# Kernel tuning notes

Hardware: AMD Instinct MI355X
Metric: run time of the kernel (lower is better)

## Reference

```python
import jax, jax.numpy as jnp
import numpy as np

B, S, D = 8, 1024, 1152
H = 16
HD = D // H
HID = int(D * 4.0)
LN_EPS = 1e-5


def layer_norm(x, w, b):
    m = jnp.mean(x, axis=-1, keepdims=True)
    v = jnp.mean(jnp.square(x - m), axis=-1, keepdims=True)
    return (x - m) * jax.lax.rsqrt(v + LN_EPS) * w + b


def modulate(x, shift, scale):
    # shift/scale: [B, D] broadcast over seq
    return x * (1.0 + scale[:, None, :]) + shift[:, None, :]


def setup_inputs() -> dict:
    key = jax.random.key(0)
    ks = jax.random.split(key, 16)
    s = 0.02
    return {
        "x": jax.random.normal(ks[0], (B, S, D), jnp.float32),
        "c": jax.random.normal(ks[1], (B, D), jnp.float32),
        "ln1_w": jnp.ones((D,), jnp.float32),
        "ln1_b": jnp.zeros((D,), jnp.float32),
        "wq": jax.random.normal(ks[2], (D, D), jnp.float32) * s,
        "wk": jax.random.normal(ks[3], (D, D), jnp.float32) * s,
        "wv": jax.random.normal(ks[4], (D, D), jnp.float32) * s,
        "wo": jax.random.normal(ks[5], (D, D), jnp.float32) * s,
        "wo_b": jnp.zeros((D,), jnp.float32),
        "ln2_w": jnp.ones((D,), jnp.float32),
        "ln2_b": jnp.zeros((D,), jnp.float32),
        "fc1_w": jax.random.normal(ks[6], (D, HID), jnp.float32) * s,
        "fc1_b": jnp.zeros((HID,), jnp.float32),
        "fc2_w": jax.random.normal(ks[7], (HID, D), jnp.float32) * s,
        "fc2_b": jnp.zeros((D,), jnp.float32),
        "ada_w": jax.random.normal(ks[8], (D, 6 * D), jnp.float32) * s,
        "ada_b": jnp.zeros((6 * D,), jnp.float32),
    }


def attention(x, wq, wk, wv, wo, wo_b):
    b, s, d = x.shape
    q = (x @ wq).reshape(b, s, H, HD).transpose(0, 2, 1, 3)  # [B,H,S,hd]
    k = (x @ wk).reshape(b, s, H, HD).transpose(0, 2, 1, 3)
    v = (x @ wv).reshape(b, s, H, HD).transpose(0, 2, 1, 3)
    scale = 1.0 / np.sqrt(HD).astype(np.float32)
    att = jnp.einsum("bhqd,bhkd->bhqk", q, k) * scale
    att = jax.nn.softmax(att, axis=-1)
    out = jnp.einsum("bhqk,bhkd->bhqd", att, v)
    out = out.transpose(0, 2, 1, 3).reshape(b, s, d)
    return out @ wo + wo_b


def reference(x, c, ln1_w, ln1_b, wq, wk, wv, wo, wo_b, ln2_w, ln2_b,
              fc1_w, fc1_b, fc2_w, fc2_b, ada_w, ada_b):
    mod = jax.nn.silu(c) @ ada_w + ada_b  # [B, 6D]
    sh_msa, sc_msa, g_msa, sh_mlp, sc_mlp, g_mlp = jnp.split(mod, 6, axis=1)
    h = modulate(layer_norm(x, ln1_w, ln1_b), sh_msa, sc_msa)
    x = x + g_msa[:, None, :] * attention(h, wq, wk, wv, wo, wo_b)
    h = modulate(layer_norm(x, ln2_w, ln2_b), sh_mlp, sc_mlp)
    h = jax.nn.gelu(h @ fc1_w + fc1_b, approximate=False) @ fc2_w + fc2_b
    x = x + g_mlp[:, None, :] * h
    return x
```

## Files before the change

kernel.cpp:

```cpp
#include <hip/hip_runtime.h>
#include <hip/hip_bf16.h>


typedef unsigned short u16;
typedef unsigned int u32;
typedef __attribute__((ext_vector_type(8))) short bf16x8;
typedef __attribute__((ext_vector_type(4))) float f32x4;
typedef __attribute__((ext_vector_type(16))) float f32x16;

#define MFMA16(a, b, c) __builtin_amdgcn_mfma_f32_16x16x32_bf16((a), (b), (c), 0, 0, 0)
#define MFMA32(a, b, c) __builtin_amdgcn_mfma_f32_32x32x16_bf16((a), (b), (c), 0, 0, 0)

__device__ __forceinline__ u16 f2bf(float f) {
  __hip_bfloat16 h = __float2bfloat16(f);
  return __builtin_bit_cast(u16, h);
}

__device__ __forceinline__ float bf2f(u16 u) {
  u32 v = ((u32)u) << 16;
  return __builtin_bit_cast(float, v);
}

__device__ __forceinline__ void gload16(const u16* g, u16* l) {
  __builtin_amdgcn_global_load_lds(
      (const __attribute__((address_space(1))) unsigned int*)(const void*)g,
      (__attribute__((address_space(3))) unsigned int*)(void*)l, 16, 0, 0);
}

__global__ __launch_bounds__(256) void k_modproj1(const float* __restrict__ cc,
                                                  const float* __restrict__ aw,
                                                  float* __restrict__ partial) {
  __shared__ float lc[8][144];
  int kc = blockIdx.y;
  for (int i = threadIdx.x; i < 1152; i += 256) {
    int b = i / 144, k = i % 144;
    float v = cc[b * 1152 + kc * 144 + k];
    lc[b][k] = v / (1.f + __expf(-v));
  }
  __syncthreads();
  int j = blockIdx.x * 256 + threadIdx.x;
  float acc[8] = {0, 0, 0, 0, 0, 0, 0, 0};
  for (int k = 0; k < 144; ++k) {
    float w = aw[(size_t)(kc * 144 + k) * 6912 + j];
    #pragma unroll
    for (int b = 0; b < 8; ++b) acc[b] += lc[b][k] * w;
  }
  #pragma unroll
  for (int b = 0; b < 8; ++b) partial[((size_t)kc * 8 + b) * 6912 + j] = acc[b];
}

__global__ __launch_bounds__(256) void k_modproj2(const float* __restrict__ partial,
                                                  const float* __restrict__ ab,
                                                  float* __restrict__ mo) {
  int j = blockIdx.x * 256 + threadIdx.x;
  float bias = ab[j];
  #pragma unroll
  for (int b = 0; b < 8; ++b) {
    float s = 0.f;
    #pragma unroll
    for (int kc = 0; kc < 8; ++kc) s += partial[((size_t)kc * 8 + b) * 6912 + j];
    mo[(size_t)b * 6912 + j] = s + bias;
  }
}

__global__ __launch_bounds__(256) void k_tcvt(const float* __restrict__ in, u16* __restrict__ out,
                                              int K, int N) {
  __shared__ float t[32][33];
  int tx = threadIdx.x & 31, ty = threadIdx.x >> 5;
  size_t bx = (size_t)blockIdx.x * 32, by = (size_t)blockIdx.y * 32;
  #pragma unroll
  for (int i = 0; i < 4; ++i) t[ty + 8 * i][tx] = in[(by + ty + 8 * i) * N + bx + tx];
  __syncthreads();
  #pragma unroll
  for (int i = 0; i < 4; ++i) out[(bx + ty + 8 * i) * K + by + tx] = f2bf(t[tx][ty + 8 * i]);
}

__global__ __launch_bounds__(256) void k_lnmod(const float* __restrict__ xin,
                                               const float* __restrict__ w,
                                               const float* __restrict__ bs,
                                               const float* __restrict__ mo,
                                               int sh_off, int sc_off, u16* __restrict__ o) {
  int row = blockIdx.x;
  int b = row >> 10;
  int tid = threadIdx.x;
  const float4* x4 = (const float4*)(xin + (size_t)row * 1152);
  float4 v0 = x4[tid];
  float4 v1 = make_float4(0.f, 0.f, 0.f, 0.f);
  if (tid < 32) v1 = x4[256 + tid];
  float s = v0.x + v0.y + v0.z + v0.w + v1.x + v1.y + v1.z + v1.w;
  float sq = v0.x * v0.x + v0.y * v0.y + v0.z * v0.z + v0.w * v0.w +
             v1.x * v1.x + v1.y * v1.y + v1.z * v1.z + v1.w * v1.w;
  #pragma unroll
  for (int d = 32; d > 0; d >>= 1) { s += __shfl_down(s, d); sq += __shfl_down(sq, d); }
  __shared__ float ps[4], pq[4];
  int wid = tid >> 6, lane = tid & 63;
  if (lane == 0) { ps[wid] = s; pq[wid] = sq; }
  __syncthreads();
  float S = ps[0] + ps[1] + ps[2] + ps[3];
  float SQ = pq[0] + pq[1] + pq[2] + pq[3];
  float mean = S * (1.f / 1152.f);
  float var = SQ * (1.f / 1152.f) - mean * mean;
  float rs = rsqrtf(var + 1e-5f);
  const float* shp = mo + (size_t)b * 6912 + sh_off;
  const float* scp = mo + (size_t)b * 6912 + sc_off;
  u16* orow = o + (size_t)row * 1152;
  {
    int col = 4 * tid;
    ushort4 u; float y;
    y = (v0.x - mean) * rs * w[col + 0] + bs[col + 0]; u.x = f2bf(y * (1.f + scp[col + 0]) + shp[col + 0]);
    y = (v0.y - mean) * rs * w[col + 1] + bs[col + 1]; u.y = f2bf(y * (1.f + scp[col + 1]) + shp[col + 1]);
    y = (v0.z - mean) * rs * w[col + 2] + bs[col + 2]; u.z = f2bf(y * (1.f + scp[col + 2]) + shp[col + 2]);
    y = (v0.w - mean) * rs * w[col + 3] + bs[col + 3]; u.w = f2bf(y * (1.f + scp[col + 3]) + shp[col + 3]);
    *(ushort4*)&orow[col] = u;
  }
  if (tid < 32) {
    int col = 1024 + 4 * tid;
    ushort4 u; float y;
    y = (v1.x - mean) * rs * w[col + 0] + bs[col + 0]; u.x = f2bf(y * (1.f + scp[col + 0]) + shp[col + 0]);
    y = (v1.y - mean) * rs * w[col + 1] + bs[col + 1]; u.y = f2bf(y * (1.f + scp[col + 1]) + shp[col + 1]);
    y = (v1.z - mean) * rs * w[col + 2] + bs[col + 2]; u.z = f2bf(y * (1.f + scp[col + 2]) + shp[col + 2]);
    y = (v1.w - mean) * rs * w[col + 3] + bs[col + 3]; u.w = f2bf(y * (1.f + scp[col + 3]) + shp[col + 3]);
    *(ushort4*)&orow[col] = u;
  }
}

template <int EPI>
__global__ __launch_bounds__(256) void k_gemm(const u16* __restrict__ A, const u16* __restrict__ Bt,
                                              int Kst, int klen, u16* __restrict__ Cb,
                                              float* __restrict__ Cf,
                                              const float* __restrict__ bias,
                                              const float* __restrict__ res,
                                              const float* __restrict__ mo, int goff,
                                              u16* __restrict__ vt) {
  const int tid = threadIdx.x;
  const int w = tid >> 6, lane = tid & 63;
  const int wr = w >> 1, wc = w & 1;
  const int l31 = lane & 31, hi = lane >> 5;

  const int nwg = gridDim.x * gridDim.y;
  const int id = blockIdx.y * gridDim.x + blockIdx.x;
  const int swz = (id & 7) * (nwg >> 3) + (id >> 3);
  const int tM = (swz / gridDim.x) * 128, tN = (swz % gridDim.x) * 128;
  const int N = gridDim.x * 128;
  const int koff = blockIdx.z * klen;

  __shared__ u16 lA[2][128 * 32];
  __shared__ u16 lB[2][128 * 32];
  f32x16 acc[2][2];
  #pragma unroll
  for (int m = 0; m < 2; ++m)
    #pragma unroll
    for (int n = 0; n < 2; ++n)
      #pragma unroll
      for (int r = 0; r < 16; ++r) acc[m][n][r] = 0.f;

  const int lrow = lane >> 2, lseg = lane & 3;
  const int fl = (lrow & 3) ^ ((lrow >> 2) & 3);
  const u16* gA = A + (size_t)(tM + w * 32 + lrow) * Kst + (lseg ^ fl) * 8 + koff;
  const u16* gB = Bt + (size_t)(tN + w * 32 + lrow) * Kst + (lseg ^ fl) * 8 + koff;
  const size_t rstep = (size_t)16 * Kst;
  const int wo0 = (w * 32) * 32, wo1 = (w * 32 + 16) * 32;
  const int fr = (l31 & 3) ^ ((l31 >> 2) & 3);
  const int c0 = (hi ^ fr) * 8;
  const int c1 = ((hi ^ fr) ^ 2) * 8;
  const int arow = (wr * 64 + l31) * 32;
  const int brow = (wc * 64 + l31) * 32;

#define STAGE(buf, ks)                        \
  do {                                        \
    gload16(gA + (ks), lA[buf] + wo0);        \
    gload16(gA + rstep + (ks), lA[buf] + wo1);\
    gload16(gB + (ks), lB[buf] + wo0);        \
    gload16(gB + rstep + (ks), lB[buf] + wo1);\
  } while (0)

#define COMPUTE(buf)                                                            \
  do {                                                                          \
    bf16x8 a00 = *(const bf16x8*)&lA[buf][arow + c0];                           \
    bf16x8 a01 = *(const bf16x8*)&lA[buf][arow + c1];                           \
    bf16x8 a10 = *(const bf16x8*)&lA[buf][arow + 1024 + c0];                    \
    bf16x8 a11 = *(const bf16x8*)&lA[buf][arow + 1024 + c1];                    \
    bf16x8 b00 = *(const bf16x8*)&lB[buf][brow + c0];                           \
    bf16x8 b01 = *(const bf16x8*)&lB[buf][brow + c1];                           \
    bf16x8 b10 = *(const bf16x8*)&lB[buf][brow + 1024 + c0];                    \
    bf16x8 b11 = *(const bf16x8*)&lB[buf][brow + 1024 + c1];                    \
    acc[0][0] = MFMA32(a00, b00, acc[0][0]);                                    \
    acc[0][1] = MFMA32(a00, b10, acc[0][1]);                                    \
    acc[1][0] = MFMA32(a10, b00, acc[1][0]);                                    \
    acc[1][1] = MFMA32(a10, b10, acc[1][1]);                                    \
    acc[0][0] = MFMA32(a01, b01, acc[0][0]);                                    \
    acc[0][1] = MFMA32(a01, b11, acc[0][1]);                                    \
    acc[1][0] = MFMA32(a11, b01, acc[1][0]);                                    \
    acc[1][1] = MFMA32(a11, b11, acc[1][1]);                                    \
  } while (0)

  const int nt = klen >> 5;
  STAGE(0, 0);
  __syncthreads();
  int t = 1;
  for (; t + 1 < nt; t += 2) {
    STAGE(1, t * 32);
    COMPUTE(0);
    __syncthreads();
    STAGE(0, t * 32 + 32);
    COMPUTE(1);
    __syncthreads();
  }
  STAGE(1, t * 32);
  COMPUTE(0);
  __syncthreads();
  COMPUTE(1);
#undef STAGE
#undef COMPUTE

  #pragma unroll
  for (int m = 0; m < 2; ++m)
    #pragma unroll
    for (int n = 0; n < 2; ++n) {
      int gcol = tN + wc * 64 + n * 32 + l31;
      #pragma unroll
      for (int q = 0; q < 4; ++q) {
        int grow0 = tM + wr * 64 + m * 32 + hi * 4 + q * 8;
        if (EPI == 3) {
          if (tN < 2304) {
            #pragma unroll
            for (int r = 0; r < 4; ++r)
              Cb[(size_t)(grow0 + r) * N + gcol] = f2bf(acc[m][n][q * 4 + r]);
          } else {
            int qq = gcol - 2304;
            int hh = qq / 72;
            int d = qq - hh * 72;
            int bb = grow0 >> 10, sl = grow0 & 1023;
            ushort4 u;
            u.x = f2bf(acc[m][n][q * 4 + 0]); u.y = f2bf(acc[m][n][q * 4 + 1]);
            u.z = f2bf(acc[m][n][q * 4 + 2]); u.w = f2bf(acc[m][n][q * 4 + 3]);
            *(ushort4*)&vt[(((size_t)bb * 16 + hh) * 72 + d) * 1024 + sl] = u;
          }
        } else if (EPI == 5) {
          u16* Po = Cb + (size_t)blockIdx.z * ((size_t)gridDim.y * 128) * N;
          #pragma unroll
          for (int r = 0; r < 4; ++r)
            Po[(size_t)(grow0 + r) * N + gcol] = f2bf(acc[m][n][q * 4 + r]);
        } else if (EPI == 1) {
          float g = mo[(size_t)(grow0 >> 10) * 6912 + goff + gcol];
          float bi = bias[gcol];
          #pragma unroll
          for (int r = 0; r < 4; ++r) {
            size_t idx = (size_t)(grow0 + r) * N + gcol;
            Cf[idx] = res[idx] + g * (acc[m][n][q * 4 + r] + bi);
          }
        } else {
          float bi = bias[gcol];
          #pragma unroll
          for (int r = 0; r < 4; ++r) {
            float z = acc[m][n][q * 4 + r] + bi;
            float z2 = z * z;
            float u = z * __fmaf_rn(z2, -0.0713548162f, -1.5957691216f);
            float e = __expf(u);
            Cb[(size_t)(grow0 + r) * N + gcol] = f2bf(z * __builtin_amdgcn_rcpf(1.f + e));
          }
        }
      }
    }
}

__global__ __launch_bounds__(256) void k_fc2red(const u16* __restrict__ p,
                                                const float* __restrict__ x1,
                                                const float* __restrict__ bias,
                                                const float* __restrict__ mo,
                                                float* __restrict__ out) {
  size_t i = ((size_t)blockIdx.x * 256 + threadIdx.x) * 4;
  int row = (int)(i / 1152);
  int col = (int)(i - (size_t)row * 1152);
  int b = row >> 10;
  ushort4 a0 = *(const ushort4*)(p + i);
  ushort4 a1 = *(const ushort4*)(p + 9437184ull + i);
  float4 r = *(const float4*)(x1 + i);
  const float* gp = mo + (size_t)b * 6912 + 5760 + col;
  const float* bp = bias + col;
  float4 o;
  o.x = r.x + gp[0] * (bf2f(a0.x) + bf2f(a1.x) + bp[0]);
  o.y = r.y + gp[1] * (bf2f(a0.y) + bf2f(a1.y) + bp[1]);
  o.z = r.z + gp[2] * (bf2f(a0.z) + bf2f(a1.z) + bp[2]);
  o.w = r.w + gp[3] * (bf2f(a0.w) + bf2f(a1.w) + bp[3]);
  *(float4*)(out + i) = o;
}

__global__ __launch_bounds__(256) void k_attn(const u16* __restrict__ QKV, const u16* __restrict__ Vt,
                                              u16* __restrict__ O) {
  const int tid = threadIdx.x;
  const int w = tid >> 6, lane = tid & 63;
  const int lr = lane & 15, kg = lane >> 4;
  int bx = blockIdx.x;
  bx = (bx & 7) * 256 + (bx >> 3);
  const int qt = bx & 15, h = (bx >> 4) & 15, b = bx >> 8;

  __shared__ u16 lQ[64][104];
  __shared__ u16 lK[64][104];
  __shared__ u16 lVt[80][72];
  __shared__ u16 lPt[4][16][72];

  const size_t qkbase = (size_t)b * 1024 * 3456 + (size_t)h * 72;
  const u16* Qg = QKV + qkbase;
  const u16* Kg = QKV + qkbase + 1152;
  const u16* Vg = Vt + ((size_t)(b * 16 + h) * 72) * 1024;

  const uint4 z4 = make_uint4(0, 0, 0, 0);
  for (int L = tid; L < 192; L += 256) {
    int r = L / 3, s = L - (L / 3) * 3;
    *(uint4*)&lQ[r][72 + s * 8] = z4;
    *(uint4*)&lK[r][72 + s * 8] = z4;
  }
  for (int L = tid; L < 72; L += 256) {
    int r = L / 9, s = L - (L / 9) * 9;
    *(uint4*)&lVt[72 + r][s * 8] = z4;
  }
  {
    int L = tid; int r = L / 9, s = L - r * 9;
    *(uint4*)&lQ[r][s * 8] = *(const uint4*)(Qg + (size_t)(qt * 64 + r) * 3456 + s * 8);
    L = tid + 256; r = L / 9; s = L - r * 9;
    *(uint4*)&lQ[r][s * 8] = *(const uint4*)(Qg + (size_t)(qt * 64 + r) * 3456 + s * 8);
    if (tid < 64) {
      L = tid + 512; r = L / 9; s = L - r * 9;
      *(uint4*)&lQ[r][s * 8] = *(const uint4*)(Qg + (size_t)(qt * 64 + r) * 3456 + s * 8);
    }
  }
  __syncthreads();

  bf16x8 bq[3];
  #pragma unroll
  for (int ks = 0; ks < 3; ++ks) bq[ks] = *(const bf16x8*)&lQ[w * 16 + lr][ks * 32 + kg * 8];

  const float scale = 0.11785113019775793f;
  float mrun = -1e30f, lrun = 0.f;
  f32x4 oacc[5];
  #pragma unroll
  for (int nd = 0; nd < 5; ++nd) oacc[nd] = f32x4{0.f, 0.f, 0.f, 0.f};

  for (int kt = 0; kt < 16; ++kt) {
    __syncthreads();
    {
      int L = tid; int r = L / 9, s = L - (L / 9) * 9;
      *(uint4*)&lK[r][s * 8] = *(const uint4*)(Kg + (size_t)(kt * 64 + r) * 3456 + s * 8);
      int d = tid >> 3, sg = tid & 7;
      *(uint4*)&lVt[d][sg * 8] = *(const uint4*)(Vg + (size_t)d * 1024 + kt * 64 + sg * 8);
      L = tid + 256; r = L / 9; s = L - r * 9;
      *(uint4*)&lK[r][s * 8] = *(const uint4*)(Kg + (size_t)(kt * 64 + r) * 3456 + s * 8);
      d = (tid + 256) >> 3; sg = tid & 7;
      *(uint4*)&lVt[d][sg * 8] = *(const uint4*)(Vg + (size_t)d * 1024 + kt * 64 + sg * 8);
      if (tid < 64) {
        L = tid + 512; r = L / 9; s = L - r * 9;
        *(uint4*)&lK[r][s * 8] = *(const uint4*)(Kg + (size_t)(kt * 64 + r) * 3456 + s * 8);
        d = (tid + 512) >> 3;
        *(uint4*)&lVt[d][sg * 8] = *(const uint4*)(Vg + (size_t)d * 1024 + kt * 64 + sg * 8);
      }
    }
    __syncthreads();

    f32x4 sfr[4];
    __builtin_amdgcn_s_setprio(1);
    #pragma unroll
    for (int kb = 0; kb < 4; ++kb) {
      f32x4 sv = f32x4{0.f, 0.f, 0.f, 0.f};
      #pragma unroll
      for (int ks = 0; ks < 3; ++ks) {
        bf16x8 ak = *(const bf16x8*)&lK[kb * 16 + lr][ks * 32 + kg * 8];
        sv = MFMA16(ak, bq[ks], sv);
      }
      sfr[kb] = sv;
    }
    __builtin_amdgcn_s_setprio(0);

    float mx = sfr[0][0];
    #pragma unroll
    for (int kb = 0; kb < 4; ++kb)
      #pragma unroll
      for (int r = 0; r < 4; ++r) mx = fmaxf(mx, sfr[kb][r]);
    mx = fmaxf(mx, __shfl_xor(mx, 16));
    mx = fmaxf(mx, __shfl_xor(mx, 32));
    mx *= scale;
    float mn = fmaxf(mrun, mx);
    float al = __expf(mrun - mn);
    mrun = mn;
    float sum = 0.f;
    #pragma unroll
    for (int kb = 0; kb < 4; ++kb) {
      #pragma unroll
      for (int rp = 0; rp < 2; ++rp) {
        float p0 = __expf(__fmaf_rn(sfr[kb][2 * rp], scale, -mn));
        float p1 = __expf(__fmaf_rn(sfr[kb][2 * rp + 1], scale, -mn));
        sum += p0 + p1;
        u32 pk = (u32)f2bf(p0) | ((u32)f2bf(p1) << 16);
        *(u32*)&lPt[w][lr][kb * 16 + kg * 4 + rp * 2] = pk;
      }
    }
    sum += __shfl_xor(sum, 16);
    sum += __shfl_xor(sum, 32);
    lrun = lrun * al + sum;
    #pragma unroll
    for (int nd = 0; nd < 5; ++nd)
      #pragma unroll
      for (int r = 0; r < 4; ++r) oacc[nd][r] *= al;

    __builtin_amdgcn_s_setprio(1);
    #pragma unroll
    for (int s = 0; s < 2; ++s) {
      bf16x8 bp = *(const bf16x8*)&lPt[w][lr][s * 32 + kg * 8];
      #pragma unroll
      for (int nd = 0; nd < 5; ++nd) {
        bf16x8 av = *(const bf16x8*)&lVt[nd * 16 + lr][s * 32 + kg * 8];
        oacc[nd] = MFMA16(av, bp, oacc[nd]);
      }
    }
    __builtin_amdgcn_s_setprio(0);
  }

  float inv = 1.f / lrun;
  size_t orow = ((size_t)b * 1024 + qt * 64 + w * 16 + lr) * 1152 + h * 72;
  #pragma unroll
  for (int nd = 0; nd < 5; ++nd) {
    int d0 = nd * 16 + kg * 4;
    if (d0 < 72) {
      ushort4 u;
      u.x = f2bf(oacc[nd][0] * inv);
      u.y = f2bf(oacc[nd][1] * inv);
      u.z = f2bf(oacc[nd][2] * inv);
      u.w = f2bf(oacc[nd][3] * inv);
      *(ushort4*)&O[orow + d0] = u;
    }
  }
}

extern "C" void kernel_launch(void* const* d_in, const int* in_sizes, int n_in,
                              void* d_out, int out_size, void* d_ws, size_t ws_size,
                              hipStream_t stream) {
  const float* x     = (const float*)d_in[0];
  const float* c     = (const float*)d_in[1];
  const float* ln1_w = (const float*)d_in[2];
  const float* ln1_b = (const float*)d_in[3];
  const float* wq    = (const float*)d_in[4];
  const float* wk    = (const float*)d_in[5];
  const float* wv    = (const float*)d_in[6];
  const float* wo    = (const float*)d_in[7];
  const float* wo_b  = (const float*)d_in[8];
  const float* ln2_w = (const float*)d_in[9];
  const float* ln2_b = (const float*)d_in[10];
  const float* fc1_w = (const float*)d_in[11];
  const float* fc1_b = (const float*)d_in[12];
  const float* fc2_w = (const float*)d_in[13];
  const float* fc2_b = (const float*)d_in[14];
  const float* ada_w = (const float*)d_in[15];
  const float* ada_b = (const float*)d_in[16];
  float* out = (float*)d_out;

  char* base = (char*)d_ws;
  size_t off = 0;
  auto alloc = [&](size_t nbytes) -> void* {
    void* p = base + off;
    off += (nbytes + 255) & ~(size_t)255;
    return p;
  };
  const size_t MD = 8192ull * 1152;
  float* partial = (float*)alloc(64ull * 6912 * 4);
  float* modb   = (float*)alloc(55296 * 4);
  u16* qkvT = (u16*)alloc(3456ull * 1152 * 2);
  u16* woT  = (u16*)alloc(1152ull * 1152 * 2);
  u16* fc1T = (u16*)alloc(4608ull * 1152 * 2);
  u16* fc2T = (u16*)alloc(1152ull * 4608 * 2);
  u16* hbuf = (u16*)alloc(MD * 2);
  float* x1 = (float*)alloc(MD * 4);
  u16* vtb  = (u16*)alloc(128ull * 72 * 1024 * 2);
  u16* fc2p = (u16*)alloc(2ull * MD * 2);
  u16* big  = (u16*)alloc(8192ull * 4608 * 2);
  u16* qkv = big;
  u16* m1 = big;

  k_modproj1<<<dim3(27, 8), 256, 0, stream>>>(c, ada_w, partial);
  k_modproj2<<<27, 256, 0, stream>>>(partial, ada_b, modb);
  k_tcvt<<<dim3(36, 36), 256, 0, stream>>>(wq, qkvT, 1152, 1152);
  k_tcvt<<<dim3(36, 36), 256, 0, stream>>>(wk, qkvT + 1152ull * 1152, 1152, 1152);
  k_tcvt<<<dim3(36, 36), 256, 0, stream>>>(wv, qkvT + 2304ull * 1152, 1152, 1152);
  k_tcvt<<<dim3(36, 36), 256, 0, stream>>>(wo, woT, 1152, 1152);
  k_tcvt<<<dim3(144, 36), 256, 0, stream>>>(fc1_w, fc1T, 1152, 4608);
  k_tcvt<<<dim3(36, 144), 256, 0, stream>>>(fc2_w, fc2T, 4608, 1152);

  k_lnmod<<<8192, 256, 0, stream>>>(x, ln1_w, ln1_b, modb, 0, 1152, hbuf);
  k_gemm<3><<<dim3(27, 64), 256, 0, stream>>>(hbuf, qkvT, 1152, 1152, qkv, nullptr, nullptr, nullptr, nullptr, 0, vtb);
  k_attn<<<2048, 256, 0, stream>>>(qkv, vtb, hbuf);
  k_gemm<1><<<dim3(9, 64), 256, 0, stream>>>(hbuf, woT, 1152, 1152, nullptr, x1, wo_b, x, modb, 2304, nullptr);
  k_lnmod<<<8192, 256, 0, stream>>>(x1, ln2_w, ln2_b, modb, 3456, 4608, hbuf);
  k_gemm<2><<<dim3(36, 64), 256, 0, stream>>>(hbuf, fc1T, 1152, 1152, m1, nullptr, fc1_b, nullptr, nullptr, 0, nullptr);
  k_gemm<5><<<dim3(9, 64, 2), 256, 0, stream>>>(m1, fc2T, 4608, 2304, fc2p, nullptr, nullptr, nullptr, nullptr, 0, nullptr);
  k_fc2red<<<9216, 256, 0, stream>>>(fc2p, x1, fc2_b, modb, out);
}
```

Before: 583.6 us.

## Widen GEMM tiles to 128x256 with each wave owning a 64-column strip

Changes the GEMM block tile from 128x128 to 128x256. Each of the four waves now computes 128 rows by 64 columns with 4x2 MFMA accumulators, which raises register use and LDS for B but improves operand reuse per LDS load. Weight buffers and the fc2 partial buffer are padded to multiples of 256 columns, and epilogues guard out-of-range columns. The wider tile halves the grid size, which may hurt wave occupancy and load balance on the narrower GEMMs. Padded weight rows are left uninitialised, but their outputs are either discarded or never read.

Result: slower. 625.1 us (+7.1%).

```diff
diff --git a/kernel.cpp b/kernel.cpp
--- a/kernel.cpp
+++ b/kernel.cpp
@@ -126,29 +126,27 @@
 
 template <int EPI>
 __global__ __launch_bounds__(256) void k_gemm(const u16* __restrict__ A, const u16* __restrict__ Bt,
-                                              int Kst, int klen, u16* __restrict__ Cb,
-                                              float* __restrict__ Cf,
+                                              int Kst, int klen, int NC,
+                                              u16* __restrict__ Cb, float* __restrict__ Cf,
                                               const float* __restrict__ bias,
                                               const float* __restrict__ res,
                                               const float* __restrict__ mo, int goff,
                                               u16* __restrict__ vt) {
   const int tid = threadIdx.x;
   const int w = tid >> 6, lane = tid & 63;
-  const int wr = w >> 1, wc = w & 1;
   const int l31 = lane & 31, hi = lane >> 5;
 
   const int nwg = gridDim.x * gridDim.y;
   const int id = blockIdx.y * gridDim.x + blockIdx.x;
   const int swz = (id & 7) * (nwg >> 3) + (id >> 3);
-  const int tM = (swz / gridDim.x) * 128, tN = (swz % gridDim.x) * 128;
-  const int N = gridDim.x * 128;
+  const int tM = (swz / gridDim.x) * 128, tN = (swz % gridDim.x) * 256;
   const int koff = blockIdx.z * klen;
 
   __shared__ u16 lA[2][128 * 32];
-  __shared__ u16 lB[2][128 * 32];
-  f32x16 acc[2][2];
-  #pragma unroll
-  for (int m = 0; m < 2; ++m)
+  __shared__ u16 lB[2][256 * 32];
+  f32x16 acc[4][2];
+  #pragma unroll
+  for (int m = 0; m < 4; ++m)
     #pragma unroll
     for (int n = 0; n < 2; ++n)
       #pragma unroll
@@ -157,41 +155,47 @@
   const int lrow = lane >> 2, lseg = lane & 3;
   const int fl = (lrow & 3) ^ ((lrow >> 2) & 3);
   const u16* gA = A + (size_t)(tM + w * 32 + lrow) * Kst + (lseg ^ fl) * 8 + koff;
-  const u16* gB = Bt + (size_t)(tN + w * 32 + lrow) * Kst + (lseg ^ fl) * 8 + koff;
+  const u16* gB = Bt + (size_t)(tN + w * 64 + lrow) * Kst + (lseg ^ fl) * 8 + koff;
   const size_t rstep = (size_t)16 * Kst;
-  const int wo0 = (w * 32) * 32, wo1 = (w * 32 + 16) * 32;
+  const int a0 = (w * 32) * 32, a1 = (w * 32 + 16) * 32;
+  const int b0 = (w * 64) * 32, b1 = (w * 64 + 16) * 32;
+  const int b2 = (w * 64 + 32) * 32, b3 = (w * 64 + 48) * 32;
   const int fr = (l31 & 3) ^ ((l31 >> 2) & 3);
   const int c0 = (hi ^ fr) * 8;
   const int c1 = ((hi ^ fr) ^ 2) * 8;
-  const int arow = (wr * 64 + l31) * 32;
-  const int brow = (wc * 64 + l31) * 32;
-
-#define STAGE(buf, ks)                        \
-  do {                                        \
-    gload16(gA + (ks), lA[buf] + wo0);        \
-    gload16(gA + rstep + (ks), lA[buf] + wo1);\
-    gload16(gB + (ks), lB[buf] + wo0);        \
-    gload16(gB + rstep + (ks), lB[buf] + wo1);\
+  const int arow = l31 * 32;
+  const int brow = (w * 64 + l31) * 32;
+
+#define STAGE(buf, ks)                                 \
+  do {                                                 \
+    gload16(gA + (ks), lA[buf] + a0);                  \
+    gload16(gA + rstep + (ks), lA[buf] + a1);          \
+    gload16(gB + (ks), lB[buf] + b0);                  \
+    gload16(gB + rstep + (ks), lB[buf] + b1);          \
+    gload16(gB + 2 * rstep + (ks), lB[buf] + b2);      \
+    gload16(gB + 3 * rstep + (ks), lB[buf] + b3);      \
   } while (0)
 
-#define COMPUTE(buf)                                                            \
-  do {                                                                          \
-    bf16x8 a00 = *(const bf16x8*)&lA[buf][arow + c0];                           \
-    bf16x8 a01 = *(const bf16x8*)&lA[buf][arow + c1];                           \
-    bf16x8 a10 = *(const bf16x8*)&lA[buf][arow + 1024 + c0];                    \
-    bf16x8 a11 = *(const bf16x8*)&lA[buf][arow + 1024 + c1];                    \
-    bf16x8 b00 = *(const bf16x8*)&lB[buf][brow + c0];                           \
-    bf16x8 b01 = *(const bf16x8*)&lB[buf][brow + c1];                           \
-    bf16x8 b10 = *(const bf16x8*)&lB[buf][brow + 1024 + c0];                    \
-    bf16x8 b11 = *(const bf16x8*)&lB[buf][brow + 1024 + c1];                    \
-    acc[0][0] = MFMA32(a00, b00, acc[0][0]);                                    \
-    acc[0][1] = MFMA32(a00, b10, acc[0][1]);                                    \
-    acc[1][0] = MFMA32(a10, b00, acc[1][0]);                                    \
-    acc[1][1] = MFMA32(a10, b10, acc[1][1]);                                    \
-    acc[0][0] = MFMA32(a01, b01, acc[0][0]);                                    \
-    acc[0][1] = MFMA32(a01, b11, acc[0][1]);                                    \
-    acc[1][0] = MFMA32(a11, b01, acc[1][0]);                                    \
-    acc[1][1] = MFMA32(a11, b11, acc[1][1]);                                    \
+#define COMPUTE(buf)                                                                 \
+  do {                                                                               \
+    bf16x8 afr[4][2], bfr[2][2];                                                     \
+    _Pragma("unroll")                                                                \
+    for (int m = 0; m < 4; ++m) {                                                    \
+      afr[m][0] = *(const bf16x8*)&lA[buf][arow + m * 1024 + c0];                    \
+      afr[m][1] = *(const bf16x8*)&lA[buf][arow + m * 1024 + c1];                    \
+    }                                                                                \
+    _Pragma("unroll")                                                                \
+    for (int n = 0; n < 2; ++n) {                                                    \
+      bfr[n][0] = *(const bf16x8*)&lB[buf][brow + n * 1024 + c0];                    \
+      bfr[n][1] = *(const bf16x8*)&lB[buf][brow + n * 1024 + c1];                    \
+    }                                                                                \
+    _Pragma("unroll")                                                                \
+    for (int m = 0; m < 4; ++m)                                                      \
+      _Pragma("unroll")                                                              \
+      for (int n = 0; n < 2; ++n) {                                                  \
+        acc[m][n] = MFMA32(afr[m][0], bfr[n][0], acc[m][n]);                         \
+        acc[m][n] = MFMA32(afr[m][1], bfr[n][1], acc[m][n]);                         \
+      }                                                                              \
   } while (0)
 
   const int nt = klen >> 5;
@@ -214,19 +218,19 @@
 #undef COMPUTE
 
   #pragma unroll
-  for (int m = 0; m < 2; ++m)
+  for (int m = 0; m < 4; ++m)
     #pragma unroll
     for (int n = 0; n < 2; ++n) {
-      int gcol = tN + wc * 64 + n * 32 + l31;
+      int gcol = tN + w * 64 + n * 32 + l31;
       #pragma unroll
       for (int q = 0; q < 4; ++q) {
-        int grow0 = tM + wr * 64 + m * 32 + hi * 4 + q * 8;
+        int grow0 = tM + m * 32 + hi * 4 + q * 8;
         if (EPI == 3) {
-          if (tN < 2304) {
+          if (gcol < 2304) {
             #pragma unroll
             for (int r = 0; r < 4; ++r)
-              Cb[(size_t)(grow0 + r) * N + gcol] = f2bf(acc[m][n][q * 4 + r]);
-          } else {
+              Cb[(size_t)(grow0 + r) * 3456 + gcol] = f2bf(acc[m][n][q * 4 + r]);
+          } else if (gcol < 3456) {
             int qq = gcol - 2304;
             int hh = qq / 72;
             int d = qq - hh * 72;
@@ -237,17 +241,19 @@
             *(ushort4*)&vt[(((size_t)bb * 16 + hh) * 72 + d) * 1024 + sl] = u;
           }
         } else if (EPI == 5) {
-          u16* Po = Cb + (size_t)blockIdx.z * ((size_t)gridDim.y * 128) * N;
+          u16* Po = Cb + (size_t)blockIdx.z * ((size_t)gridDim.y * 128) * NC;
           #pragma unroll
           for (int r = 0; r < 4; ++r)
-            Po[(size_t)(grow0 + r) * N + gcol] = f2bf(acc[m][n][q * 4 + r]);
+            Po[(size_t)(grow0 + r) * NC + gcol] = f2bf(acc[m][n][q * 4 + r]);
         } else if (EPI == 1) {
-          float g = mo[(size_t)(grow0 >> 10) * 6912 + goff + gcol];
-          float bi = bias[gcol];
-          #pragma unroll
-          for (int r = 0; r < 4; ++r) {
-            size_t idx = (size_t)(grow0 + r) * N + gcol;
-            Cf[idx] = res[idx] + g * (acc[m][n][q * 4 + r] + bi);
+          if (gcol < 1152) {
+            float g = mo[(size_t)(grow0 >> 10) * 6912 + goff + gcol];
+            float bi = bias[gcol];
+            #pragma unroll
+            for (int r = 0; r < 4; ++r) {
+              size_t idx = (size_t)(grow0 + r) * 1152 + gcol;
+              Cf[idx] = res[idx] + g * (acc[m][n][q * 4 + r] + bi);
+            }
           }
         } else {
           float bi = bias[gcol];
@@ -257,7 +263,7 @@
             float z2 = z * z;
             float u = z * __fmaf_rn(z2, -0.0713548162f, -1.5957691216f);
             float e = __expf(u);
-            Cb[(size_t)(grow0 + r) * N + gcol] = f2bf(z * __builtin_amdgcn_rcpf(1.f + e));
+            Cb[(size_t)(grow0 + r) * NC + gcol] = f2bf(z * __builtin_amdgcn_rcpf(1.f + e));
           }
         }
       }
@@ -273,8 +279,9 @@
   int row = (int)(i / 1152);
   int col = (int)(i - (size_t)row * 1152);
   int b = row >> 10;
-  ushort4 a0 = *(const ushort4*)(p + i);
-  ushort4 a1 = *(const ushort4*)(p + 9437184ull + i);
+  size_t pi = (size_t)row * 1280 + col;
+  ushort4 a0 = *(const ushort4*)(p + pi);
+  ushort4 a1 = *(const ushort4*)(p + 10485760ull + pi);
   float4 r = *(const float4*)(x1 + i);
   const float* gp = mo + (size_t)b * 6912 + 5760 + col;
   const float* bp = bias + col;
@@ -463,14 +470,14 @@
   const size_t MD = 8192ull * 1152;
   float* partial = (float*)alloc(64ull * 6912 * 4);
   float* modb   = (float*)alloc(55296 * 4);
-  u16* qkvT = (u16*)alloc(3456ull * 1152 * 2);
-  u16* woT  = (u16*)alloc(1152ull * 1152 * 2);
+  u16* qkvT = (u16*)alloc(3584ull * 1152 * 2);
+  u16* woT  = (u16*)alloc(1280ull * 1152 * 2);
   u16* fc1T = (u16*)alloc(4608ull * 1152 * 2);
-  u16* fc2T = (u16*)alloc(1152ull * 4608 * 2);
+  u16* fc2T = (u16*)alloc(1280ull * 4608 * 2);
   u16* hbuf = (u16*)alloc(MD * 2);
   float* x1 = (float*)alloc(MD * 4);
   u16* vtb  = (u16*)alloc(128ull * 72 * 1024 * 2);
-  u16* fc2p = (u16*)alloc(2ull * MD * 2);
+  u16* fc2p = (u16*)alloc(2ull * 8192 * 1280 * 2);
   u16* big  = (u16*)alloc(8192ull * 4608 * 2);
   u16* qkv = big;
   u16* m1 = big;
@@ -485,11 +492,11 @@
   k_tcvt<<<dim3(36, 144), 256, 0, stream>>>(fc2_w, fc2T, 4608, 1152);
 
   k_lnmod<<<8192, 256, 0, stream>>>(x, ln1_w, ln1_b, modb, 0, 1152, hbuf);
-  k_gemm<3><<<dim3(27, 64), 256, 0, stream>>>(hbuf, qkvT, 1152, 1152, qkv, nullptr, nullptr, nullptr, nullptr, 0, vtb);
+  k_gemm<3><<<dim3(14, 64), 256, 0, stream>>>(hbuf, qkvT, 1152, 1152, 3456, qkv, nullptr, nullptr, nullptr, nullptr, 0, vtb);
   k_attn<<<2048, 256, 0, stream>>>(qkv, vtb, hbuf);
-  k_gemm<1><<<dim3(9, 64), 256, 0, stream>>>(hbuf, woT, 1152, 1152, nullptr, x1, wo_b, x, modb, 2304, nullptr);
+  k_gemm<1><<<dim3(5, 64), 256, 0, stream>>>(hbuf, woT, 1152, 1152, 1280, nullptr, x1, wo_b, x, modb, 2304, nullptr);
   k_lnmod<<<8192, 256, 0, stream>>>(x1, ln2_w, ln2_b, modb, 3456, 4608, hbuf);
-  k_gemm<2><<<dim3(36, 64), 256, 0, stream>>>(hbuf, fc1T, 1152, 1152, m1, nullptr, fc1_b, nullptr, nullptr, 0, nullptr);
-  k_gemm<5><<<dim3(9, 64, 2), 256, 0, stream>>>(m1, fc2T, 4608, 2304, fc2p, nullptr, nullptr, nullptr, nullptr, 0, nullptr);
+  k_gemm<2><<<dim3(18, 64), 256, 0, stream>>>(hbuf, fc1T, 1152, 1152, 4608, m1, nullptr, fc1_b, nullptr, nullptr, 0, nullptr);
+  k_gemm<5><<<dim3(5, 64, 2), 256, 0, stream>>>(m1, fc2T, 4608, 2304, 1280, fc2p, nullptr, nullptr, nullptr, nullptr, 0, nullptr);
   k_fc2red<<<9216, 256, 0, stream>>>(fc2p, x1, fc2_b, modb, out);
 }
```

## Triple-buffer GEMM LDS staging with vmcnt-based waits and MFMA priority

Applied to the files above, without the earlier changes.

Moves the bf16 GEMM main loop from double to triple buffering in LDS. Explicit s_waitcnt vmcnt plus a raw barrier replaces __syncthreads, so two tiles of global loads stay in flight while one is computed. s_setprio raises wave priority around the MFMA block. This costs 50% more LDS per block, which may reduce occupancy. The loop now assumes the K tile count is a multiple of three, and correctness relies on each stage being exactly four async loads.

After: 581.3 us. About the same (-0.4%).

```diff
diff --git a/kernel.cpp b/kernel.cpp
--- a/kernel.cpp
+++ b/kernel.cpp
@@ -144,8 +144,8 @@
   const int N = gridDim.x * 128;
   const int koff = blockIdx.z * klen;
 
-  __shared__ u16 lA[2][128 * 32];
-  __shared__ u16 lB[2][128 * 32];
+  __shared__ u16 lA[3][128 * 32];
+  __shared__ u16 lB[3][128 * 32];
   f32x16 acc[2][2];
   #pragma unroll
   for (int m = 0; m < 2; ++m)
@@ -184,6 +184,7 @@
     bf16x8 b01 = *(const bf16x8*)&lB[buf][brow + c1];                           \
     bf16x8 b10 = *(const bf16x8*)&lB[buf][brow + 1024 + c0];                    \
     bf16x8 b11 = *(const bf16x8*)&lB[buf][brow + 1024 + c1];                    \
+    __builtin_amdgcn_s_setprio(1);                                              \
     acc[0][0] = MFMA32(a00, b00, acc[0][0]);                                    \
     acc[0][1] = MFMA32(a00, b10, acc[0][1]);                                    \
     acc[1][0] = MFMA32(a10, b00, acc[1][0]);                                    \
@@ -192,26 +193,32 @@
     acc[0][1] = MFMA32(a01, b11, acc[0][1]);                                    \
     acc[1][0] = MFMA32(a11, b01, acc[1][0]);                                    \
     acc[1][1] = MFMA32(a11, b11, acc[1][1]);                                    \
+    __builtin_amdgcn_s_setprio(0);                                              \
+  } while (0)
+
+#define WAITBAR(Nst)                                          \
+  do {                                                        \
+    asm volatile("s_waitcnt vmcnt(" #Nst ")" ::: "memory");   \
+    __builtin_amdgcn_s_barrier();                             \
+    __builtin_amdgcn_sched_barrier(0);                        \
   } while (0)
 
   const int nt = klen >> 5;
   STAGE(0, 0);
-  __syncthreads();
-  int t = 1;
-  for (; t + 1 < nt; t += 2) {
-    STAGE(1, t * 32);
-    COMPUTE(0);
-    __syncthreads();
-    STAGE(0, t * 32 + 32);
-    COMPUTE(1);
-    __syncthreads();
-  }
-  STAGE(1, t * 32);
-  COMPUTE(0);
-  __syncthreads();
-  COMPUTE(1);
+  STAGE(1, 32);
+  int ks = 64;
+  for (int g = 0; g < nt / 3 - 1; ++g) {
+    WAITBAR(4); STAGE(2, ks);      COMPUTE(0);
+    WAITBAR(4); STAGE(0, ks + 32); COMPUTE(1);
+    WAITBAR(4); STAGE(1, ks + 64); COMPUTE(2);
+    ks += 96;
+  }
+  WAITBAR(4); STAGE(2, ks); COMPUTE(0);
+  WAITBAR(4); COMPUTE(1);
+  WAITBAR(0); COMPUTE(2);
 #undef STAGE
 #undef COMPUTE
+#undef WAITBAR
 
   #pragma unroll
   for (int m = 0; m < 2; ++m)
```
